# Kernel tuning notes

Measured on AMD Instinct MI355X. Metric: run time of the kernel, lower is better.

The kernel has to match this reference:

```python
import jax, jax.numpy as jnp
import numpy as np
import math

DIM = 1024
HEAD = 16


def setup_inputs() -> dict:
    key = jax.random.key(0)
    k1, k2, k3, k4, k5 = jax.random.split(key, 5)
    scale = 1.0 / math.sqrt(DIM)
    return {
        "x": jax.random.normal(k1, (2, 2048, DIM), dtype=jnp.float32),
        "W_kqv": jax.random.uniform(k2, (3 * DIM, DIM), minval=-scale, maxval=scale, dtype=jnp.float32),
        "b_kqv": jax.random.uniform(k3, (3 * DIM,), minval=-scale, maxval=scale, dtype=jnp.float32),
        "W_out": jax.random.uniform(k4, (DIM, DIM), minval=-scale, maxval=scale, dtype=jnp.float32),
        "b_out": jax.random.uniform(k5, (DIM,), minval=-scale, maxval=scale, dtype=jnp.float32),
    }


def reference(x, W_kqv, b_kqv, W_out, b_out):
    b, s, h = x.shape
    head = HEAD
    d = h // head
    # fused QKV projection (torch Linear: x @ W.T + b)
    kqv = jnp.einsum("bsh,oh->bso", x, W_kqv) + b_kqv  # [b, s, 3h]
    q, k, v = jnp.split(kqv, 3, axis=-1)
    # [b, s, h] -> [b, head, s, d]
    q = q.reshape(b, s, head, d).transpose(0, 2, 1, 3)
    k = k.reshape(b, s, head, d).transpose(0, 2, 1, 3)
    v = v.reshape(b, s, head, d).transpose(0, 2, 1, 3)
    scores = jnp.einsum("bnqd,bnkd->bnqk", q, k) / jnp.sqrt(jnp.float32(d))
    attn = jax.nn.softmax(scores, axis=-1)
    ctx = jnp.einsum("bnqk,bnkd->bnqd", attn, v)  # [b, head, s, d]
    ctx = ctx.transpose(0, 2, 1, 3).reshape(b, s, h)
    return jnp.einsum("bsh,oh->bso", ctx, W_out) + b_out
```

## Files before the change

kernel.cpp:

```cpp
#include <hip/hip_runtime.h>
#include <hip/hip_bf16.h>

#define DIM   1024
#define NHEAD 16
#define HD    64
#define SEQ   2048
#define BATCH 2
#define QKV3  3072

using short8 = __attribute__((ext_vector_type(8))) short;
using f32x4  = __attribute__((ext_vector_type(4))) float;

__device__ inline short f2bf(float f) {
    union { float f; unsigned u; } x; x.f = f;
    const unsigned r = (x.u + 0x7FFFu + ((x.u >> 16) & 1u)) >> 16;
    return (short)r;
}
__device__ inline unsigned pkbf(float a, float b) {
    union { __hip_bfloat162 h; unsigned u; } cv;
    cv.h = __float22bfloat162_rn(make_float2(a, b));
    return cv.u;
}

__device__ __forceinline__ void g2l16(const void* gptr, void* ldsbase) {
    __builtin_amdgcn_global_load_lds(
        (const __attribute__((address_space(1))) unsigned int*)(unsigned long long)gptr,
        (__attribute__((address_space(3))) unsigned int*)(unsigned int)(unsigned long long)ldsbase,
        16, 0, 0);
}

__global__ __launch_bounds__(256)
void conv_bf16(const float* __restrict__ x, const float* __restrict__ wk,
               const float* __restrict__ wo,
               unsigned short* __restrict__ xb, unsigned short* __restrict__ wkb,
               unsigned short* __restrict__ wob)
{
    const int bid = blockIdx.x;
    const float* src; unsigned short* dst; size_t base;
    if (bid < 1024)      { src = x;  dst = xb;  base = (size_t)bid * 4096; }
    else if (bid < 1792) { src = wk; dst = wkb; base = (size_t)(bid - 1024) * 4096; }
    else                 { src = wo; dst = wob; base = (size_t)(bid - 1792) * 4096; }
    const size_t off = base + threadIdx.x * 16;
    const float4 f0 = *(const float4*)(src + off + 0);
    const float4 f1 = *(const float4*)(src + off + 4);
    const float4 f2 = *(const float4*)(src + off + 8);
    const float4 f3 = *(const float4*)(src + off + 12);
    uint4 o0, o1;
    o0.x = pkbf(f0.x, f0.y); o0.y = pkbf(f0.z, f0.w);
    o0.z = pkbf(f1.x, f1.y); o0.w = pkbf(f1.z, f1.w);
    o1.x = pkbf(f2.x, f2.y); o1.y = pkbf(f2.z, f2.w);
    o1.z = pkbf(f3.x, f3.y); o1.w = pkbf(f3.z, f3.w);
    *(uint4*)(dst + off + 0) = o0;
    *(uint4*)(dst + off + 8) = o1;
}

__global__ __launch_bounds__(256)
void gemm_qkv(const unsigned short* __restrict__ A, const unsigned short* __restrict__ B,
              const float* __restrict__ bias,
              unsigned short* __restrict__ qbf, unsigned short* __restrict__ kbf,
              unsigned short* __restrict__ vtbf)
{
    constexpr int BK = 32;
    const int K = DIM;
    __shared__ short As[128 * BK];
    __shared__ short Bs[128 * BK];

    const int tid  = threadIdx.x;
    const int lane = tid & 63;
    const int wave = tid >> 6;
    const int quad = lane >> 4;
    const int ln   = lane & 15;
    const int wm   = (wave & 1) * 64;
    const int wn   = (wave >> 1) * 64;

    const int bid = blockIdx.x;
    const int xcd = bid & 7;
    const int t   = bid >> 3;
    const int m0  = (xcd * 4 + (t & 3)) * 128;
    const int n0  = (t >> 2) * 128;

    int srow[2], sg[2];
#pragma unroll
    for (int i = 0; i < 2; ++i) {
        const int c  = wave * 128 + i * 64 + lane;
        srow[i] = c >> 2;
        sg[i]   = (c & 3) ^ ((srow[i] >> 1) & 3);
    }

    f32x4 acc[4][4];
#pragma unroll
    for (int i = 0; i < 4; ++i)
#pragma unroll
        for (int j = 0; j < 4; ++j) acc[i][j] = (f32x4){0.f, 0.f, 0.f, 0.f};

    for (int k0 = 0; k0 < K; k0 += BK) {
        __syncthreads();
#pragma unroll
        for (int i = 0; i < 2; ++i) {
            const int cb = wave * 128 + i * 64;
            g2l16(A + (size_t)(m0 + srow[i]) * K + k0 + sg[i] * 8, &As[cb * 8]);
            g2l16(B + (size_t)(n0 + srow[i]) * K + k0 + sg[i] * 8, &Bs[cb * 8]);
        }
        __syncthreads();

        short8 a[4], b[4];
#pragma unroll
        for (int i = 0; i < 4; ++i) {
            const int row = wm + i * 16 + ln;
            const int ch  = quad ^ ((row >> 1) & 3);
            a[i] = *(const short8*)&As[row * BK + ch * 8];
        }
#pragma unroll
        for (int j = 0; j < 4; ++j) {
            const int row = wn + j * 16 + ln;
            const int ch  = quad ^ ((row >> 1) & 3);
            b[j] = *(const short8*)&Bs[row * BK + ch * 8];
        }
#pragma unroll
        for (int i = 0; i < 4; ++i)
#pragma unroll
            for (int j = 0; j < 4; ++j)
                acc[i][j] = __builtin_amdgcn_mfma_f32_16x16x32_bf16(
                    a[i], b[j], acc[i][j], 0, 0, 0);
    }

#pragma unroll
    for (int j = 0; j < 4; ++j) {
        const int col = n0 + wn + j * 16 + ln;
        const int sel = col >> 10;
        const int c   = col & 1023;
        const int hh  = c >> 6;
        const int dd  = c & 63;
        const float bv = bias[col];
        if (sel < 2) {
            unsigned short* dst = (sel == 0) ? qbf : kbf;
            const float qs = (sel == 0) ? 0.125f : 1.0f;
#pragma unroll
            for (int i = 0; i < 4; ++i)
#pragma unroll
                for (int r2 = 0; r2 < 4; ++r2) {
                    const int row = m0 + wm + i * 16 + quad * 4 + r2;
                    const int bb = row >> 11, ss = row & 2047;
                    dst[((size_t)(bb * NHEAD + hh) * SEQ + ss) * HD + dd] =
                        (unsigned short)f2bf((acc[i][j][r2] + bv) * qs);
                }
        } else {
            const int row0 = m0 + wm + quad * 4;
            const int bb = row0 >> 11;
            const size_t vbase = ((size_t)(bb * NHEAD + hh) * HD + dd) * SEQ;
#pragma unroll
            for (int i = 0; i < 4; ++i) {
                const int ss0 = (row0 & 2047) + i * 16;
                uint2 pk;
                pk.x = pkbf(acc[i][j][0] + bv, acc[i][j][1] + bv);
                pk.y = pkbf(acc[i][j][2] + bv, acc[i][j][3] + bv);
                *(uint2*)&vtbf[vbase + ss0] = pk;
            }
        }
    }
}

__global__ __launch_bounds__(256)
void attn_flash_mfma(const unsigned short* __restrict__ qbf,
                     const unsigned short* __restrict__ kbf,
                     const unsigned short* __restrict__ vtbf,
                     unsigned short* __restrict__ ctxbf)
{
    constexpr int LDK = 72, LDV = 72, LDP = 72;
    __shared__ short Ks[64 * LDK];
    __shared__ short Vt[64 * LDV];
    __shared__ short Ps[128 * LDP];
    __shared__ float Lq[128];

    const int tid  = threadIdx.x;
    const int lane = tid & 63;
    const int wave = tid >> 6;
    const int quad = lane >> 4;
    const int ln   = lane & 15;

    const int qt = blockIdx.x & 15;
    const int h  = (blockIdx.x >> 4) & 15;
    const int b  = blockIdx.x >> 8;
    const int q0 = qt * 128;

    const size_t sbase = ((size_t)(b * NHEAD + h)) * SEQ * HD;
    const size_t vbase = ((size_t)(b * NHEAD + h)) * HD * SEQ;

#pragma unroll
    for (int it = 0; it < 4; ++it) {
        const int ch = tid + it * 256;
        const int r  = ch >> 3;
        const int cc = ch & 7;
        *(short8*)&Ps[r * LDP + cc * 8] =
            *(const short8*)&qbf[sbase + (size_t)(q0 + r) * HD + cc * 8];
    }
    __syncthreads();
    short8 qf[2][2];
#pragma unroll
    for (int sm = 0; sm < 2; ++sm)
#pragma unroll
        for (int kc = 0; kc < 2; ++kc)
            qf[sm][kc] = *(const short8*)&Ps[(wave * 32 + sm * 16 + ln) * LDP + kc * 32 + quad * 8];

    f32x4 O[2][4];
#pragma unroll
    for (int sm = 0; sm < 2; ++sm)
#pragma unroll
        for (int dj = 0; dj < 4; ++dj) O[sm][dj] = (f32x4){0.f, 0.f, 0.f, 0.f};
    float lsum[2] = {0.f, 0.f};

    short8 kr[2], vr[2];
#pragma unroll
    for (int it = 0; it < 2; ++it) {
        const int ch = tid + it * 256;
        const int r  = ch >> 3;
        const int cc = ch & 7;
        kr[it] = *(const short8*)&kbf[sbase + (size_t)r * HD + cc * 8];
        vr[it] = *(const short8*)&vtbf[vbase + (size_t)r * SEQ + cc * 8];
    }

    for (int kt = 0; kt < SEQ / 64; ++kt) {
        __syncthreads();
#pragma unroll
        for (int it = 0; it < 2; ++it) {
            const int ch = tid + it * 256;
            const int r  = ch >> 3;
            const int cc = ch & 7;
            *(short8*)&Ks[r * LDK + cc * 8] = kr[it];
            *(short8*)&Vt[r * LDV + cc * 8] = vr[it];
        }
        if (kt + 1 < SEQ / 64) {
            const int k0n = (kt + 1) * 64;
#pragma unroll
            for (int it = 0; it < 2; ++it) {
                const int ch = tid + it * 256;
                const int r  = ch >> 3;
                const int cc = ch & 7;
                kr[it] = *(const short8*)&kbf[sbase + (size_t)(k0n + r) * HD + cc * 8];
                vr[it] = *(const short8*)&vtbf[vbase + (size_t)r * SEQ + k0n + cc * 8];
            }
        }
        __syncthreads();

        f32x4 st[2][4];
#pragma unroll
        for (int j = 0; j < 4; ++j) {
            const short8 kf0 = *(const short8*)&Ks[(j * 16 + ln) * LDK + quad * 8];
            const short8 kf1 = *(const short8*)&Ks[(j * 16 + ln) * LDK + 32 + quad * 8];
#pragma unroll
            for (int sm = 0; sm < 2; ++sm) {
                f32x4 tt = __builtin_amdgcn_mfma_f32_16x16x32_bf16(
                    kf0, qf[sm][0], (f32x4){0.f, 0.f, 0.f, 0.f}, 0, 0, 0);
                st[sm][j] = __builtin_amdgcn_mfma_f32_16x16x32_bf16(
                    kf1, qf[sm][1], tt, 0, 0, 0);
            }
        }

#pragma unroll
        for (int sm = 0; sm < 2; ++sm) {
#pragma unroll
            for (int j = 0; j < 4; ++j) {
                const float p0 = __expf(st[sm][j][0]);
                const float p1 = __expf(st[sm][j][1]);
                const float p2 = __expf(st[sm][j][2]);
                const float p3 = __expf(st[sm][j][3]);
                lsum[sm] += (p0 + p1) + (p2 + p3);
                uint2 pk;
                pk.x = pkbf(p0, p1);
                pk.y = pkbf(p2, p3);
                *(uint2*)&Ps[(wave * 32 + sm * 16 + ln) * LDP + j * 16 + quad * 4] = pk;
            }
        }

#pragma unroll
        for (int kc = 0; kc < 2; ++kc) {
            const short8 pf0 = *(const short8*)&Ps[(wave * 32 + ln) * LDP + kc * 32 + quad * 8];
            const short8 pf1 = *(const short8*)&Ps[(wave * 32 + 16 + ln) * LDP + kc * 32 + quad * 8];
#pragma unroll
            for (int dj = 0; dj < 4; ++dj) {
                const short8 vf = *(const short8*)&Vt[(dj * 16 + ln) * LDV + kc * 32 + quad * 8];
                O[0][dj] = __builtin_amdgcn_mfma_f32_16x16x32_bf16(pf0, vf, O[0][dj], 0, 0, 0);
                O[1][dj] = __builtin_amdgcn_mfma_f32_16x16x32_bf16(pf1, vf, O[1][dj], 0, 0, 0);
            }
        }
    }

    lsum[0] += __shfl_xor(lsum[0], 16); lsum[0] += __shfl_xor(lsum[0], 32);
    lsum[1] += __shfl_xor(lsum[1], 16); lsum[1] += __shfl_xor(lsum[1], 32);
    Lq[wave * 32 + ln]      = lsum[0];
    Lq[wave * 32 + 16 + ln] = lsum[1];
    __syncthreads();

#pragma unroll
    for (int sm = 0; sm < 2; ++sm)
#pragma unroll
        for (int r2 = 0; r2 < 4; ++r2) {
            const float inv = 1.0f / Lq[wave * 32 + sm * 16 + quad * 4 + r2];
            const int row = b * SEQ + q0 + wave * 32 + sm * 16 + quad * 4 + r2;
#pragma unroll
            for (int dj = 0; dj < 4; ++dj)
                ctxbf[(size_t)row * DIM + h * HD + dj * 16 + ln] =
                    (unsigned short)f2bf(O[sm][dj][r2] * inv);
        }
}

__global__ __launch_bounds__(256)
void gemm_out(const unsigned short* __restrict__ A, const unsigned short* __restrict__ B,
              const float* __restrict__ bias, float* __restrict__ C)
{
    constexpr int BK = 32;
    const int K = DIM, N = DIM;
    __shared__ short As[128 * BK];
    __shared__ short Bs[64 * BK];

    const int tid  = threadIdx.x;
    const int lane = tid & 63;
    const int wave = tid >> 6;
    const int quad = lane >> 4;
    const int ln   = lane & 15;
    const int wm   = (wave & 1) * 64;
    const int wn   = (wave >> 1) * 32;

    const int bid = blockIdx.x;
    const int xcd = bid & 7;
    const int t   = bid >> 3;
    const int m0  = (xcd * 4 + (t & 3)) * 128;
    const int n0  = (t >> 2) * 64;

    int srow[2], sg[2];
#pragma unroll
    for (int i = 0; i < 2; ++i) {
        const int c  = wave * 128 + i * 64 + lane;
        srow[i] = c >> 2;
        sg[i]   = (c & 3) ^ ((srow[i] >> 1) & 3);
    }
    const int cB  = wave * 64 + lane;
    const int brow = cB >> 2;
    const int bg   = (cB & 3) ^ ((brow >> 1) & 3);

    f32x4 acc[4][2];
#pragma unroll
    for (int i = 0; i < 4; ++i)
#pragma unroll
        for (int j = 0; j < 2; ++j) acc[i][j] = (f32x4){0.f, 0.f, 0.f, 0.f};

    for (int k0 = 0; k0 < K; k0 += BK) {
        __syncthreads();
#pragma unroll
        for (int i = 0; i < 2; ++i)
            g2l16(A + (size_t)(m0 + srow[i]) * K + k0 + sg[i] * 8,
                  &As[(wave * 128 + i * 64) * 8]);
        g2l16(B + (size_t)(n0 + brow) * K + k0 + bg * 8, &Bs[(wave * 64) * 8]);
        __syncthreads();

        short8 a[4], b[2];
#pragma unroll
        for (int i = 0; i < 4; ++i) {
            const int row = wm + i * 16 + ln;
            const int ch  = quad ^ ((row >> 1) & 3);
            a[i] = *(const short8*)&As[row * BK + ch * 8];
        }
#pragma unroll
        for (int j = 0; j < 2; ++j) {
            const int row = wn + j * 16 + ln;
            const int ch  = quad ^ ((row >> 1) & 3);
            b[j] = *(const short8*)&Bs[row * BK + ch * 8];
        }
#pragma unroll
        for (int i = 0; i < 4; ++i)
#pragma unroll
            for (int j = 0; j < 2; ++j)
                acc[i][j] = __builtin_amdgcn_mfma_f32_16x16x32_bf16(
                    a[i], b[j], acc[i][j], 0, 0, 0);
    }

#pragma unroll
    for (int j = 0; j < 2; ++j) {
        const int col = n0 + wn + j * 16 + ln;
        const float bv = bias[col];
#pragma unroll
        for (int i = 0; i < 4; ++i)
#pragma unroll
            for (int r2 = 0; r2 < 4; ++r2) {
                const int row = m0 + wm + i * 16 + quad * 4 + r2;
                C[(size_t)row * N + col] = acc[i][j][r2] + bv;
            }
    }
}

extern "C" void kernel_launch(void* const* d_in, const int* in_sizes, int n_in,
                              void* d_out, int out_size, void* d_ws, size_t ws_size,
                              hipStream_t stream)
{
    const float* x     = (const float*)d_in[0];
    const float* W_kqv = (const float*)d_in[1];
    const float* b_kqv = (const float*)d_in[2];
    const float* W_out = (const float*)d_in[3];
    const float* b_out = (const float*)d_in[4];
    float* out = (float*)d_out;

    char* w = (char*)d_ws;
    unsigned short* qbf   = (unsigned short*)w;  w += (size_t)BATCH * NHEAD * SEQ * HD * 2;
    unsigned short* kbf   = (unsigned short*)w;  w += (size_t)BATCH * NHEAD * SEQ * HD * 2;
    unsigned short* vtbf  = (unsigned short*)w;  w += (size_t)BATCH * NHEAD * HD * SEQ * 2;
    unsigned short* ctxbf = (unsigned short*)w;  w += (size_t)BATCH * SEQ * DIM * 2;
    unsigned short* xb    = (unsigned short*)w;  w += (size_t)BATCH * SEQ * DIM * 2;
    unsigned short* wkb   = (unsigned short*)w;  w += (size_t)QKV3 * DIM * 2;
    unsigned short* wob   = (unsigned short*)w;

    dim3 blk(256);

    conv_bf16<<<dim3(2048), blk, 0, stream>>>(x, W_kqv, W_out, xb, wkb, wob);

    gemm_qkv<<<dim3(768), blk, 0, stream>>>(xb, wkb, b_kqv, qbf, kbf, vtbf);

    attn_flash_mfma<<<dim3(BATCH * NHEAD * (SEQ / 128)), blk, 0, stream>>>(
        qbf, kbf, vtbf, ctxbf);

    gemm_out<<<dim3(512), blk, 0, stream>>>(ctxbf, wob, b_out, out);
}
```

Baseline: 204.7 us.

## Double-buffer K/V via direct global-to-LDS loads with swizzle and MFMA row sums

The attention kernel now loads K and V tiles straight from global memory into double-buffered, XOR-swizzled LDS with g2l16, replacing the register staging and padded rows, and drops one barrier per iteration. The softmax row sums are computed by an MFMA against a ones vector instead of scalar adds and shuffles. Exponentials use exp2 with log2(e) folded into the Q scale. Block order is remapped so that consecutive blocks cover different heads. The aim is to overlap loads with compute and cut VALU and LDS bank-conflict overhead, at the cost of more LDS and some extra MFMA work.

```diff
diff --git a/kernel.cpp b/kernel.cpp
--- a/kernel.cpp
+++ b/kernel.cpp
@@ -134,7 +134,7 @@
         const float bv = bias[col];
         if (sel < 2) {
             unsigned short* dst = (sel == 0) ? qbf : kbf;
-            const float qs = (sel == 0) ? 0.125f : 1.0f;
+            const float qs = (sel == 0) ? 0.18033688f : 1.0f;
 #pragma unroll
             for (int i = 0; i < 4; ++i)
 #pragma unroll
@@ -166,11 +166,10 @@
                      const unsigned short* __restrict__ vtbf,
                      unsigned short* __restrict__ ctxbf)
 {
-    constexpr int LDK = 72, LDV = 72, LDP = 72;
-    __shared__ short Ks[64 * LDK];
-    __shared__ short Vt[64 * LDV];
+    constexpr int LDP = 72;
+    __shared__ short Ks[2][64 * 64];
+    __shared__ short Vt[2][64 * 64];
     __shared__ short Ps[128 * LDP];
-    __shared__ float Lq[128];
 
     const int tid  = threadIdx.x;
     const int lane = tid & 63;
@@ -178,13 +177,23 @@
     const int quad = lane >> 4;
     const int ln   = lane & 15;
 
-    const int qt = blockIdx.x & 15;
-    const int h  = (blockIdx.x >> 4) & 15;
-    const int b  = blockIdx.x >> 8;
-    const int q0 = qt * 128;
-
-    const size_t sbase = ((size_t)(b * NHEAD + h)) * SEQ * HD;
-    const size_t vbase = ((size_t)(b * NHEAD + h)) * HD * SEQ;
+    const int bid = blockIdx.x;
+    const int bh  = bid & 31;
+    const int qt  = bid >> 5;
+    const int q0  = qt * 128;
+    const int b   = bh >> 4;
+    const int h   = bh & 15;
+
+    const size_t sbase = (size_t)bh * SEQ * HD;
+    const size_t vbase = (size_t)bh * HD * SEQ;
+
+    int srw[2], scg[2];
+#pragma unroll
+    for (int it = 0; it < 2; ++it) {
+        const int ch = tid + it * 256;
+        srw[it] = ch >> 3;
+        scg[it] = (ch & 7) ^ (srw[it] & 7);
+    }
 
 #pragma unroll
     for (int it = 0; it < 4; ++it) {
@@ -194,7 +203,14 @@
         *(short8*)&Ps[r * LDP + cc * 8] =
             *(const short8*)&qbf[sbase + (size_t)(q0 + r) * HD + cc * 8];
     }
+#pragma unroll
+    for (int it = 0; it < 2; ++it) {
+        const int cb = tid + it * 256;
+        g2l16(kbf + sbase + (size_t)srw[it] * HD + scg[it] * 8, &Ks[0][cb * 8]);
+        g2l16(vtbf + vbase + (size_t)srw[it] * SEQ + scg[it] * 8, &Vt[0][cb * 8]);
+    }
     __syncthreads();
+
     short8 qf[2][2];
 #pragma unroll
     for (int sm = 0; sm < 2; ++sm)
@@ -207,46 +223,36 @@
     for (int sm = 0; sm < 2; ++sm)
 #pragma unroll
         for (int dj = 0; dj < 4; ++dj) O[sm][dj] = (f32x4){0.f, 0.f, 0.f, 0.f};
-    float lsum[2] = {0.f, 0.f};
-
-    short8 kr[2], vr[2];
-#pragma unroll
-    for (int it = 0; it < 2; ++it) {
-        const int ch = tid + it * 256;
-        const int r  = ch >> 3;
-        const int cc = ch & 7;
-        kr[it] = *(const short8*)&kbf[sbase + (size_t)r * HD + cc * 8];
-        vr[it] = *(const short8*)&vtbf[vbase + (size_t)r * SEQ + cc * 8];
-    }
+    f32x4 lacc[2];
+    lacc[0] = (f32x4){0.f, 0.f, 0.f, 0.f};
+    lacc[1] = (f32x4){0.f, 0.f, 0.f, 0.f};
+
+    short8 vone;
+#pragma unroll
+    for (int t = 0; t < 8; ++t) vone[t] = (short)0x3F80;
 
     for (int kt = 0; kt < SEQ / 64; ++kt) {
-        __syncthreads();
-#pragma unroll
-        for (int it = 0; it < 2; ++it) {
-            const int ch = tid + it * 256;
-            const int r  = ch >> 3;
-            const int cc = ch & 7;
-            *(short8*)&Ks[r * LDK + cc * 8] = kr[it];
-            *(short8*)&Vt[r * LDV + cc * 8] = vr[it];
-        }
+        const int p = kt & 1;
         if (kt + 1 < SEQ / 64) {
             const int k0n = (kt + 1) * 64;
 #pragma unroll
             for (int it = 0; it < 2; ++it) {
-                const int ch = tid + it * 256;
-                const int r  = ch >> 3;
-                const int cc = ch & 7;
-                kr[it] = *(const short8*)&kbf[sbase + (size_t)(k0n + r) * HD + cc * 8];
-                vr[it] = *(const short8*)&vtbf[vbase + (size_t)r * SEQ + k0n + cc * 8];
-            }
-        }
-        __syncthreads();
+                const int cb = tid + it * 256;
+                g2l16(kbf + sbase + (size_t)(k0n + srw[it]) * HD + scg[it] * 8,
+                      &Ks[1 - p][cb * 8]);
+                g2l16(vtbf + vbase + (size_t)srw[it] * SEQ + k0n + scg[it] * 8,
+                      &Vt[1 - p][cb * 8]);
+            }
+        }
 
         f32x4 st[2][4];
 #pragma unroll
         for (int j = 0; j < 4; ++j) {
-            const short8 kf0 = *(const short8*)&Ks[(j * 16 + ln) * LDK + quad * 8];
-            const short8 kf1 = *(const short8*)&Ks[(j * 16 + ln) * LDK + 32 + quad * 8];
+            const int row = j * 16 + ln;
+            const int c0 = quad ^ (row & 7);
+            const int c1 = (4 + quad) ^ (row & 7);
+            const short8 kf0 = *(const short8*)&Ks[p][row * 64 + c0 * 8];
+            const short8 kf1 = *(const short8*)&Ks[p][row * 64 + c1 * 8];
 #pragma unroll
             for (int sm = 0; sm < 2; ++sm) {
                 f32x4 tt = __builtin_amdgcn_mfma_f32_16x16x32_bf16(
@@ -257,45 +263,42 @@
         }
 
 #pragma unroll
-        for (int sm = 0; sm < 2; ++sm) {
+        for (int sm = 0; sm < 2; ++sm)
 #pragma unroll
             for (int j = 0; j < 4; ++j) {
-                const float p0 = __expf(st[sm][j][0]);
-                const float p1 = __expf(st[sm][j][1]);
-                const float p2 = __expf(st[sm][j][2]);
-                const float p3 = __expf(st[sm][j][3]);
-                lsum[sm] += (p0 + p1) + (p2 + p3);
+                const float p0 = __builtin_amdgcn_exp2f(st[sm][j][0]);
+                const float p1 = __builtin_amdgcn_exp2f(st[sm][j][1]);
+                const float p2 = __builtin_amdgcn_exp2f(st[sm][j][2]);
+                const float p3 = __builtin_amdgcn_exp2f(st[sm][j][3]);
                 uint2 pk;
                 pk.x = pkbf(p0, p1);
                 pk.y = pkbf(p2, p3);
                 *(uint2*)&Ps[(wave * 32 + sm * 16 + ln) * LDP + j * 16 + quad * 4] = pk;
             }
-        }
 
 #pragma unroll
         for (int kc = 0; kc < 2; ++kc) {
             const short8 pf0 = *(const short8*)&Ps[(wave * 32 + ln) * LDP + kc * 32 + quad * 8];
             const short8 pf1 = *(const short8*)&Ps[(wave * 32 + 16 + ln) * LDP + kc * 32 + quad * 8];
+            lacc[0] = __builtin_amdgcn_mfma_f32_16x16x32_bf16(pf0, vone, lacc[0], 0, 0, 0);
+            lacc[1] = __builtin_amdgcn_mfma_f32_16x16x32_bf16(pf1, vone, lacc[1], 0, 0, 0);
 #pragma unroll
             for (int dj = 0; dj < 4; ++dj) {
-                const short8 vf = *(const short8*)&Vt[(dj * 16 + ln) * LDV + kc * 32 + quad * 8];
+                const int row = dj * 16 + ln;
+                const int cg  = (kc * 4 + quad) ^ (row & 7);
+                const short8 vf = *(const short8*)&Vt[p][row * 64 + cg * 8];
                 O[0][dj] = __builtin_amdgcn_mfma_f32_16x16x32_bf16(pf0, vf, O[0][dj], 0, 0, 0);
                 O[1][dj] = __builtin_amdgcn_mfma_f32_16x16x32_bf16(pf1, vf, O[1][dj], 0, 0, 0);
             }
         }
-    }
-
-    lsum[0] += __shfl_xor(lsum[0], 16); lsum[0] += __shfl_xor(lsum[0], 32);
-    lsum[1] += __shfl_xor(lsum[1], 16); lsum[1] += __shfl_xor(lsum[1], 32);
-    Lq[wave * 32 + ln]      = lsum[0];
-    Lq[wave * 32 + 16 + ln] = lsum[1];
-    __syncthreads();
+        __syncthreads();
+    }
 
 #pragma unroll
     for (int sm = 0; sm < 2; ++sm)
 #pragma unroll
         for (int r2 = 0; r2 < 4; ++r2) {
-            const float inv = 1.0f / Lq[wave * 32 + sm * 16 + quad * 4 + r2];
+            const float inv = 1.0f / lacc[sm][r2];
             const int row = b * SEQ + q0 + wave * 32 + sm * 16 + quad * 4 + r2;
 #pragma unroll
             for (int dj = 0; dj < 4; ++dj)
@@ -414,8 +417,7 @@
 
     gemm_qkv<<<dim3(768), blk, 0, stream>>>(xb, wkb, b_kqv, qbf, kbf, vtbf);
 
-    attn_flash_mfma<<<dim3(BATCH * NHEAD * (SEQ / 128)), blk, 0, stream>>>(
-        qbf, kbf, vtbf, ctxbf);
+    attn_flash_mfma<<<dim3(512), blk, 0, stream>>>(qbf, kbf, vtbf, ctxbf);
 
     gemm_out<<<dim3(512), blk, 0, stream>>>(ctxbf, wob, b_out, out);
 }
```

New measurement: 205.3 us. No clear change (+0.3%).
